# Kernel optimization log

Measured on AMD Instinct MI355X. Metric: run time of the kernel, lower is better.

The kernel has to match this reference:

```python
import jax, jax.numpy as jnp
import numpy as np

HEAD_DIM = 64
N_HEADS = 16
DIM = 1024
EPS = 1e-6
GRID = 32  # make_axial_pos(32, 32)


def _make_theta(head_dim=HEAD_DIM, n_heads=N_HEADS):
    hd8 = head_dim // 8
    nh2 = n_heads // 2
    freqs = np.exp(np.linspace(np.log(np.pi), np.log(10 * np.pi), hd8 * nh2 + 1)[:-1])
    freqs = freqs.reshape(hd8, nh2).T  # (nh2, hd8)
    # axial positions on a 32x32 grid, cell centers in [-1, 1]
    p = np.linspace(-1.0, 1.0, GRID + 1)
    p = (p[:-1] + p[1:]) / 2
    pos = np.stack(np.meshgrid(p, p, indexing='ij'), axis=-1).reshape(GRID * GRID, 2)
    pos = np.concatenate([np.zeros((1, 2)), pos], axis=0)  # (1025, 2)
    th1 = np.concatenate([pos[:-1, None, 0:1] * freqs, pos[:-1, None, 1:2] * freqs], axis=-1)
    th2 = np.concatenate([pos[1:, None, 0:1] * freqs, pos[1:, None, 1:2] * freqs], axis=-1)
    # (seq=1024, n_heads, head_dim//4)
    return np.concatenate([th1, th2], axis=1).astype(np.float32)


def setup_inputs() -> dict:
    key = jax.random.key(0)
    k1, k2, k3 = jax.random.split(key, 3)
    B, S = 8, 1024
    x = jax.random.normal(k1, (B, S, DIM), dtype=jnp.float32)
    scale = jnp.ones((DIM,), dtype=jnp.float32)
    w_qkv = jax.random.normal(k2, (3 * DIM, DIM), dtype=jnp.float32) * 0.02
    w_out = jax.random.normal(k3, (DIM, DIM), dtype=jnp.float32) * 0.02
    theta = jnp.asarray(_make_theta())
    return {"x": x, "scale": scale, "w_qkv": w_qkv, "w_out": w_out, "theta": theta}


def _rms_norm(x, scale, eps):
    xf = x.astype(jnp.float32)
    mean_sq = jnp.mean(xf * xf, axis=-1, keepdims=True)
    s = scale.astype(jnp.float32) * jax.lax.rsqrt(mean_sq + eps)
    return x * s.astype(x.dtype)


def _rope(x, theta):
    # x: (B, H, S, D); theta: (H, S, d) with d = D // 4 -> rotates first D//2 dims
    d = theta.shape[-1]
    cos = jnp.cos(theta)
    sin = jnp.sin(theta)
    x1, x2, rest = x[..., :d], x[..., d:2 * d], x[..., 2 * d:]
    y1 = x1 * cos - x2 * sin
    y2 = x2 * cos + x1 * sin
    return jnp.concatenate([y1, y2, rest], axis=-1)


def reference(x, scale, w_qkv, w_out, theta):
    B, S, dim = x.shape
    H = N_HEADS
    D = dim // H
    skip = x
    xn = _rms_norm(x, scale, EPS)
    qkv = xn @ w_qkv.T                                  # (B, S, 3*dim)
    qkv = qkv.reshape(B, S, 3, H, D).transpose(0, 3, 2, 1, 4)  # (B, H, 3, S, D)
    q, k, v = qkv[:, :, 0], qkv[:, :, 1], qkv[:, :, 2]  # (B, H, S, D)
    th = theta[:S].transpose(1, 0, 2)                   # (H, S, D//4)
    q = _rope(q, th)
    k = _rope(k, th)
    scores = jnp.einsum('bhsd,bhtd->bhst', q, k) / jnp.sqrt(jnp.float32(D))
    causal = jnp.tril(jnp.ones((S, S), dtype=bool))
    scores = jnp.where(causal, scores, jnp.finfo(scores.dtype).min)
    attn = jax.nn.softmax(scores, axis=-1)
    o = jnp.einsum('bhst,bhtd->bhsd', attn, v)          # (B, H, S, D)
    o = o.transpose(0, 2, 1, 3).reshape(B, S, dim)
    return o @ w_out.T + skip
```

## Files before the change

### kernel.cpp

```cpp
#include <hip/hip_runtime.h>
#include <hip/hip_bf16.h>
#include <cstdint>

typedef short short8 __attribute__((ext_vector_type(8)));
typedef float f32x4 __attribute__((ext_vector_type(4)));

#define MFMA16(a, b, c) __builtin_amdgcn_mfma_f32_16x16x32_bf16((a), (b), (c), 0, 0, 0)

__device__ __forceinline__ unsigned short f2b(float f) {
    __hip_bfloat16 h = __float2bfloat16(f);
    return __builtin_bit_cast(unsigned short, h);
}

__device__ __forceinline__ void gl_lds16(const void* g, void* l) {
    __builtin_amdgcn_global_load_lds((const __attribute__((address_space(1))) void*)g,
                                     (__attribute__((address_space(3))) void*)l, 16, 0, 0);
}

#define QSC 0.18033688011112042f

__global__ void rmsnorm_kernel(const float* __restrict__ x, const float* __restrict__ scale,
                               unsigned short* __restrict__ xn) {
    const int row = blockIdx.x;
    const int tid = threadIdx.x;
    const float4* xr = (const float4*)(x + (size_t)row * 1024);
    float4 vx = xr[tid];
    float ss = vx.x * vx.x + vx.y * vx.y + vx.z * vx.z + vx.w * vx.w;
#pragma unroll
    for (int m = 1; m < 64; m <<= 1) ss += __shfl_xor(ss, m);
    __shared__ float wsum[4];
    if ((tid & 63) == 0) wsum[tid >> 6] = ss;
    __syncthreads();
    float tot = wsum[0] + wsum[1] + wsum[2] + wsum[3];
    float rs = rsqrtf(tot * (1.0f / 1024.0f) + 1e-6f);
    const float4* sr = (const float4*)scale;
    float4 sv = sr[tid];
    ushort4 r;
    r.x = f2b(vx.x * sv.x * rs);
    r.y = f2b(vx.y * sv.y * rs);
    r.z = f2b(vx.z * sv.z * rs);
    r.w = f2b(vx.w * sv.w * rs);
    *(ushort4*)(xn + (size_t)row * 1024 + tid * 4) = r;
}

__global__ void f2b_kernel(const float* __restrict__ in, unsigned short* __restrict__ outp, int n4) {
    int i = blockIdx.x * 256 + threadIdx.x;
    if (i < n4) {
        float4 vv = ((const float4*)in)[i];
        ushort4 r;
        r.x = f2b(vv.x);
        r.y = f2b(vv.y);
        r.z = f2b(vv.z);
        r.w = f2b(vv.w);
        ((ushort4*)outp)[i] = r;
    }
}

constexpr int BM = 128, BN = 128, BK = 64, KDIM = 1024, NT = KDIM / BK;

template <int EPI>
__launch_bounds__(256, 4) __global__
    void gemm_bt(const unsigned short* __restrict__ A, const unsigned short* __restrict__ Bw,
                 unsigned short* __restrict__ qo, unsigned short* __restrict__ ko,
                 unsigned short* __restrict__ vo, const float* __restrict__ skip,
                 float* __restrict__ out, const float* __restrict__ theta) {
    __shared__ unsigned short As[BM * BK];
    __shared__ unsigned short Bs[BN * BK];
    const int tid = threadIdx.x;
    const int lane = tid & 63, w = tid >> 6;
    const int wr = w >> 1, wc = w & 1;
    const int lr = lane & 15, lg = lane >> 4;
    constexpr int NBX = (EPI == 0) ? 24 : 8;
    const int f = blockIdx.x;
    const int xcd = f & 7, wloc = f >> 3;
    const int g = xcd * (NBX * 8) + wloc;
    const int bx = g % NBX, by = g / NBX;
    const int m0 = by * BM;
    const int n0 = bx * BN;
    const int NCOL = (EPI == 0) ? 3072 : 1024;

    f32x4 acc[4][4] = {};

    auto stage = [&](int kt) {
        const int k0 = kt * BK;
#pragma unroll
        for (int i = 0; i < 4; ++i) {
            int seg = i * 256 + tid;
            int row = seg >> 3, c8 = (seg & 7) ^ (row & 7);
            gl_lds16(A + (size_t)(m0 + row) * KDIM + k0 + c8 * 8, &As[(i * 256 + w * 64) * 8]);
            gl_lds16(Bw + (size_t)(n0 + row) * KDIM + k0 + c8 * 8, &Bs[(i * 256 + w * 64) * 8]);
        }
    };

    for (int kt = 0; kt < NT; ++kt) {
        stage(kt);
        __syncthreads();
#pragma unroll
        for (int kkc = 0; kkc < 2; ++kkc) {
            short8 a[4], b[4];
            const int slot = ((kkc * 4 + lg) ^ (lr & 7)) * 8;
#pragma unroll
            for (int m = 0; m < 4; ++m)
                a[m] = *(const short8*)&As[(wr * 64 + m * 16 + lr) * BK + slot];
#pragma unroll
            for (int n = 0; n < 4; ++n)
                b[n] = *(const short8*)&Bs[(wc * 64 + n * 16 + lr) * BK + slot];
#pragma unroll
            for (int m = 0; m < 4; ++m)
#pragma unroll
                for (int n = 0; n < 4; ++n) acc[m][n] = MFMA16(a[m], b[n], acc[m][n]);
        }
        __syncthreads();
    }

    if (EPI == 0) {
        const int colb = n0 + wc * 64;
        const int c = colb >> 10, h = (colb >> 6) & 15;
#pragma unroll
        for (int m = 0; m < 4; ++m) {
            int grow0 = m0 + wr * 64 + m * 16 + lg * 4;
            int b = grow0 >> 10, s0 = grow0 & 1023;
            if (c == 2) {
#pragma unroll
                for (int n = 0; n < 4; ++n) {
                    int d = n * 16 + lr;
                    ushort4 r;
                    r.x = f2b(acc[m][n][0]);
                    r.y = f2b(acc[m][n][1]);
                    r.z = f2b(acc[m][n][2]);
                    r.w = f2b(acc[m][n][3]);
                    *(ushort4*)&vo[(((size_t)(b * 16 + h)) * 64 + d) * 1024 + s0] = r;
                }
            } else {
                unsigned short* dst = (c == 0) ? qo : ko;
                float sc = (c == 0) ? QSC : 1.0f;
#pragma unroll
                for (int j = 0; j < 4; ++j) {
                    int s = s0 + j;
                    float th = theta[((s * 16 + h) << 4) + lr];
                    float sn, cs;
                    __sincosf(th, &sn, &cs);
                    float x1 = acc[m][0][j], x2 = acc[m][1][j];
                    size_t rowb = (((size_t)(b * 16 + h)) * 1024 + s) * 64;
                    dst[rowb + lr]      = f2b((x1 * cs - x2 * sn) * sc);
                    dst[rowb + 16 + lr] = f2b((x2 * cs + x1 * sn) * sc);
                    dst[rowb + 32 + lr] = f2b(acc[m][2][j] * sc);
                    dst[rowb + 48 + lr] = f2b(acc[m][3][j] * sc);
                }
            }
        }
    } else {
#pragma unroll
        for (int m = 0; m < 4; ++m)
#pragma unroll
            for (int n = 0; n < 4; ++n) {
                int gcol = n0 + wc * 64 + n * 16 + lr;
#pragma unroll
                for (int j = 0; j < 4; ++j) {
                    int grow = m0 + wr * 64 + m * 16 + lg * 4 + j;
                    size_t idx = (size_t)grow * NCOL + gcol;
                    out[idx] = acc[m][n][j] + skip[idx];
                }
            }
    }
}

__launch_bounds__(256, 4) __global__
    void attn_kernel(const unsigned short* __restrict__ q, const unsigned short* __restrict__ k,
                     const unsigned short* __restrict__ vt, unsigned short* __restrict__ o) {
    constexpr int S = 1024, D = 64;
    __shared__ unsigned short Ks[2][64 * 64];
    __shared__ unsigned short Vs[2][64 * 64];
    __shared__ unsigned Pls[4][16 * 32];
    const int tid = threadIdx.x, lane = tid & 63, w = tid >> 6;
    const int lr = lane & 15, lg = lane >> 4;
    const int f = blockIdx.x;
    const int r0 = f & 127;
    const int qb = 7 - (f >> 7);
    const int bh = (r0 & 7) * 16 + (r0 >> 3);
    const int qs = qb * 128;
    const size_t base = (size_t)bh * (S * D);
    const int wrow0 = qs + w * 32;

    short8 qf[2][2];
#pragma unroll
    for (int m = 0; m < 2; ++m) {
        const unsigned short* qp = q + base + (size_t)(wrow0 + m * 16 + lr) * D;
        qf[m][0] = *(const short8*)(qp + lg * 8);
        qf[m][1] = *(const short8*)(qp + 32 + lg * 8);
    }

    f32x4 of[2][4] = {};
    float mrun[2] = {-1e30f, -1e30f};
    float lrun[2] = {0.f, 0.f};

    const int nkt = 2 * qb + 2;

    auto stageK = [&](int buf, int kt) {
#pragma unroll
        for (int i = 0; i < 2; ++i) {
            int seg = i * 256 + tid;
            int row = seg >> 3, c8 = (seg & 7) ^ (row & 7);
            gl_lds16(k + base + (size_t)(kt * 64 + row) * D + c8 * 8,
                     &Ks[buf][(i * 256 + w * 64) * 8]);
        }
    };
    auto stageV = [&](int buf, int kt) {
#pragma unroll
        for (int i = 0; i < 2; ++i) {
            int seg = i * 256 + tid;
            int row = seg >> 3, c8 = (seg & 7) ^ (row & 7);
            gl_lds16(vt + base + (size_t)row * S + kt * 64 + c8 * 8,
                     &Vs[buf][(i * 256 + w * 64) * 8]);
        }
    };

    unsigned* Pw = &Pls[w][0];
    const int swz = (lr & 3) << 3;

    stageK(0, 0);
    stageV(0, 0);
    __syncthreads();

    for (int kt = 0; kt < nkt; ++kt) {
        const int b = kt & 1;
        if (kt + 1 < nkt) {
            stageK(b ^ 1, kt + 1);
            stageV(b ^ 1, kt + 1);
        }

        if (kt * 64 <= wrow0 + 31) {
            f32x4 sf[2][4] = {};
            __builtin_amdgcn_s_setprio(1);
#pragma unroll
            for (int n = 0; n < 4; ++n) {
                const int r = n * 16 + lr;
#pragma unroll
                for (int kkc = 0; kkc < 2; ++kkc) {
                    short8 kf = *(const short8*)&Ks[b][r * 64 + (((kkc * 4 + lg) ^ (lr & 7)) * 8)];
#pragma unroll
                    for (int m = 0; m < 2; ++m) sf[m][n] = MFMA16(kf, qf[m][kkc], sf[m][n]);
                }
            }
            __builtin_amdgcn_s_setprio(0);

            if (kt * 64 + 63 > wrow0) {
#pragma unroll
                for (int m = 0; m < 2; ++m)
#pragma unroll
                    for (int n = 0; n < 4; ++n)
#pragma unroll
                        for (int j = 0; j < 4; ++j) {
                            int t = kt * 64 + 16 * n + lg * 4 + j;
                            int qr = wrow0 + m * 16 + lr;
                            if (t > qr) sf[m][n][j] = -1e30f;
                        }
            }

#pragma unroll
            for (int m = 0; m < 2; ++m) {
                float mx = -1e30f;
#pragma unroll
                for (int n = 0; n < 4; ++n)
                    mx = fmaxf(mx, fmaxf(fmaxf(sf[m][n][0], sf[m][n][1]),
                                         fmaxf(sf[m][n][2], sf[m][n][3])));
                mx = fmaxf(mx, __shfl_xor(mx, 16));
                mx = fmaxf(mx, __shfl_xor(mx, 32));

                if (__any(mx > mrun[m] + 8.0f)) {
                    float newm = fmaxf(mrun[m], mx);
                    float sc = __builtin_amdgcn_exp2f(mrun[m] - newm);
                    mrun[m] = newm;
                    float psum = 0.f;
#pragma unroll
                    for (int n = 0; n < 4; ++n)
#pragma unroll
                        for (int j = 0; j < 4; ++j) {
                            float p = __builtin_amdgcn_exp2f(sf[m][n][j] - newm);
                            sf[m][n][j] = p;
                            psum += p;
                        }
                    lrun[m] = lrun[m] * sc + psum;
#pragma unroll
                    for (int n2 = 0; n2 < 4; ++n2) of[m][n2] *= sc;
                } else {
                    float mo = mrun[m];
                    float psum = 0.f;
#pragma unroll
                    for (int n = 0; n < 4; ++n)
#pragma unroll
                        for (int j = 0; j < 4; ++j) {
                            float p = __builtin_amdgcn_exp2f(sf[m][n][j] - mo);
                            sf[m][n][j] = p;
                            psum += p;
                        }
                    lrun[m] += psum;
                }
            }

            short8 pa[2][2];
#pragma unroll
            for (int m = 0; m < 2; ++m) {
                unsigned Dk[4][2];
#pragma unroll
                for (int n = 0; n < 4; ++n)
#pragma unroll
                    for (int w2 = 0; w2 < 2; ++w2)
                        Dk[n][w2] = (unsigned)f2b(sf[m][n][2 * w2]) |
                                    ((unsigned)f2b(sf[m][n][2 * w2 + 1]) << 16);
#pragma unroll
                for (int n = 0; n < 4; ++n)
#pragma unroll
                    for (int w2 = 0; w2 < 2; ++w2)
                        Pw[lr * 32 + ((8 * n + 2 * lg + w2) ^ swz)] = Dk[n][w2];
#pragma unroll
                for (int kkc = 0; kkc < 2; ++kkc)
                    pa[m][kkc] = *(const short8*)&Pw[lr * 32 + ((kkc * 16 + 4 * lg) ^ swz)];
            }

            __builtin_amdgcn_s_setprio(1);
#pragma unroll
            for (int kkc = 0; kkc < 2; ++kkc) {
#pragma unroll
                for (int n2 = 0; n2 < 4; ++n2) {
                    const int r = n2 * 16 + lr;
                    short8 bv = *(const short8*)&Vs[b][r * 64 + (((kkc * 4 + lg) ^ (lr & 7)) * 8)];
#pragma unroll
                    for (int m = 0; m < 2; ++m) of[m][n2] = MFMA16(pa[m][kkc], bv, of[m][n2]);
                }
            }
            __builtin_amdgcn_s_setprio(0);
        }

        __syncthreads();
    }

    float* Lw = (float*)&Pls[w][0];
#pragma unroll
    for (int m = 0; m < 2; ++m) {
        float l = lrun[m];
        l += __shfl_xor(l, 16);
        l += __shfl_xor(l, 32);
        Lw[m * 16 + lr] = l;
    }
    const int bb = bh >> 4, h = bh & 15;
#pragma unroll
    for (int m = 0; m < 2; ++m)
#pragma unroll
        for (int j = 0; j < 4; ++j) {
            float inv = 1.f / Lw[m * 16 + lg * 4 + j];
            int srow = wrow0 + m * 16 + lg * 4 + j;
            size_t ob = ((size_t)(bb * 1024 + srow)) * 1024 + h * 64;
#pragma unroll
            for (int n2 = 0; n2 < 4; ++n2)
                o[ob + n2 * 16 + lr] = f2b(of[m][n2][j] * inv);
        }
}

extern "C" void kernel_launch(void* const* d_in, const int* in_sizes, int n_in, void* d_out,
                              int out_size, void* d_ws, size_t ws_size, hipStream_t stream) {
    const float* x = (const float*)d_in[0];
    const float* scale = (const float*)d_in[1];
    const float* w_qkv = (const float*)d_in[2];
    const float* w_out = (const float*)d_in[3];
    const float* theta = (const float*)d_in[4];
    float* out = (float*)d_out;

    char* p = (char*)d_ws;
    unsigned short* xn = (unsigned short*)p;      p += (size_t)8192 * 1024 * 2;
    unsigned short* wqb = (unsigned short*)p;     p += (size_t)3072 * 1024 * 2;
    unsigned short* wob = (unsigned short*)p;     p += (size_t)1024 * 1024 * 2;
    unsigned short* qb_ = (unsigned short*)p;     p += (size_t)128 * 1024 * 64 * 2;
    unsigned short* kb_ = (unsigned short*)p;     p += (size_t)128 * 1024 * 64 * 2;
    unsigned short* vb_ = (unsigned short*)p;     p += (size_t)128 * 1024 * 64 * 2;
    unsigned short* ob_ = (unsigned short*)p;     p += (size_t)8192 * 1024 * 2;

    rmsnorm_kernel<<<8192, 256, 0, stream>>>(x, scale, xn);
    f2b_kernel<<<3072, 256, 0, stream>>>(w_qkv, wqb, 786432);
    f2b_kernel<<<1024, 256, 0, stream>>>(w_out, wob, 262144);
    gemm_bt<0><<<1536, 256, 0, stream>>>(xn, wqb, qb_, kb_, vb_, nullptr, nullptr, theta);
    attn_kernel<<<1024, 256, 0, stream>>>(qb_, kb_, vb_, ob_);
    gemm_bt<1><<<512, 256, 0, stream>>>(ob_, wob, nullptr, nullptr, nullptr, x, out, nullptr);
}
```

Baseline: 161.4 us.

## Stage attention output through LDS for vector stores and rebalance causal block order

The attention epilogue now writes the normalized output tile into shared memory reused from the K/V buffers, then emits 16-byte vector stores per row instead of scattered 2-byte stores. The causal query-block order is permuted so heavy and light blocks interleave across the grid. The P-tile swizzle pattern is also changed to reduce LDS bank conflicts. It relies on all waves being done with the K/V buffers before reuse. The final loop ends with a __syncthreads, so that holds.

```diff
diff --git a/kernel.cpp b/kernel.cpp
--- a/kernel.cpp
+++ b/kernel.cpp
@@ -169,15 +169,14 @@
     void attn_kernel(const unsigned short* __restrict__ q, const unsigned short* __restrict__ k,
                      const unsigned short* __restrict__ vt, unsigned short* __restrict__ o) {
     constexpr int S = 1024, D = 64;
-    __shared__ unsigned short Ks[2][64 * 64];
-    __shared__ unsigned short Vs[2][64 * 64];
+    __shared__ unsigned short KVs[4][4096];
     __shared__ unsigned Pls[4][16 * 32];
     const int tid = threadIdx.x, lane = tid & 63, w = tid >> 6;
     const int lr = lane & 15, lg = lane >> 4;
     const int f = blockIdx.x;
-    const int r0 = f & 127;
-    const int qb = 7 - (f >> 7);
-    const int bh = (r0 & 7) * 16 + (r0 >> 3);
+    constexpr int qmap[8] = {7, 6, 0, 1, 5, 4, 2, 3};
+    const int qb = qmap[f >> 7];
+    const int bh = (f & 7) * 16 + ((f >> 3) & 15);
     const int qs = qb * 128;
     const size_t base = (size_t)bh * (S * D);
     const int wrow0 = qs + w * 32;
@@ -202,7 +201,7 @@
             int seg = i * 256 + tid;
             int row = seg >> 3, c8 = (seg & 7) ^ (row & 7);
             gl_lds16(k + base + (size_t)(kt * 64 + row) * D + c8 * 8,
-                     &Ks[buf][(i * 256 + w * 64) * 8]);
+                     &KVs[buf][(i * 256 + w * 64) * 8]);
         }
     };
     auto stageV = [&](int buf, int kt) {
@@ -211,12 +210,12 @@
             int seg = i * 256 + tid;
             int row = seg >> 3, c8 = (seg & 7) ^ (row & 7);
             gl_lds16(vt + base + (size_t)row * S + kt * 64 + c8 * 8,
-                     &Vs[buf][(i * 256 + w * 64) * 8]);
+                     &KVs[2 + buf][(i * 256 + w * 64) * 8]);
         }
     };
 
     unsigned* Pw = &Pls[w][0];
-    const int swz = (lr & 3) << 3;
+    const int swz = (lr & 7) << 2;
 
     stageK(0, 0);
     stageV(0, 0);
@@ -237,7 +236,8 @@
                 const int r = n * 16 + lr;
 #pragma unroll
                 for (int kkc = 0; kkc < 2; ++kkc) {
-                    short8 kf = *(const short8*)&Ks[b][r * 64 + (((kkc * 4 + lg) ^ (lr & 7)) * 8)];
+                    short8 kf =
+                        *(const short8*)&KVs[b][r * 64 + (((kkc * 4 + lg) ^ (lr & 7)) * 8)];
 #pragma unroll
                     for (int m = 0; m < 2; ++m) sf[m][n] = MFMA16(kf, qf[m][kkc], sf[m][n]);
                 }
@@ -324,7 +324,8 @@
 #pragma unroll
                 for (int n2 = 0; n2 < 4; ++n2) {
                     const int r = n2 * 16 + lr;
-                    short8 bv = *(const short8*)&Vs[b][r * 64 + (((kkc * 4 + lg) ^ (lr & 7)) * 8)];
+                    short8 bv =
+                        *(const short8*)&KVs[2 + b][r * 64 + (((kkc * 4 + lg) ^ (lr & 7)) * 8)];
 #pragma unroll
                     for (int m = 0; m < 2; ++m) of[m][n2] = MFMA16(pa[m][kkc], bv, of[m][n2]);
                 }
@@ -343,18 +344,26 @@
         l += __shfl_xor(l, 32);
         Lw[m * 16 + lr] = l;
     }
+
+    unsigned short* Ts = &KVs[0][0] + w * 2304;
     const int bb = bh >> 4, h = bh & 15;
 #pragma unroll
     for (int m = 0; m < 2; ++m)
 #pragma unroll
         for (int j = 0; j < 4; ++j) {
             float inv = 1.f / Lw[m * 16 + lg * 4 + j];
-            int srow = wrow0 + m * 16 + lg * 4 + j;
-            size_t ob = ((size_t)(bb * 1024 + srow)) * 1024 + h * 64;
+            int row = m * 16 + lg * 4 + j;
 #pragma unroll
             for (int n2 = 0; n2 < 4; ++n2)
-                o[ob + n2 * 16 + lr] = f2b(of[m][n2][j] * inv);
-        }
+                Ts[row * 72 + n2 * 16 + lr] = f2b(of[m][n2][j] * inv);
+        }
+#pragma unroll
+    for (int i = 0; i < 4; ++i) {
+        int row = i * 8 + lg * 2 + (lr >> 3);
+        short8 v = *(const short8*)&Ts[row * 72 + (lr & 7) * 8];
+        size_t ob = ((size_t)(bb * 1024 + wrow0 + row)) * 1024 + h * 64 + (lr & 7) * 8;
+        *(short8*)&o[ob] = v;
+    }
 }
 
 extern "C" void kernel_launch(void* const* d_in, const int* in_sizes, int n_in, void* d_out,
```

Measured after the change: 164.9 us. 1.02x slower.
